# Performance work log

Hardware: AMD Instinct MI355X
Metric: run time of the kernel (lower is better)

## Reference

```python
import jax, jax.numpy as jnp
import numpy as np

M1, M2, BS = 2000, 400, 8
AT = M1 + M2
E1, E2, E3 = 60000, 20000, 20000
H, F, NG, L, C = 64, 64, 50, 4, 4
CUTOFF = 10.0
LOG2 = 0.6931471805599453  # shift of ShiftedSoftplus


def _ssp(x):
    return jax.nn.softplus(x) - LOG2


def _smear(d):
    # GaussianSmearing(0, cutoff, NG)
    offset = jnp.linspace(0.0, CUTOFF, NG)
    coeff = -0.5 / (offset[1] - offset[0]) ** 2
    return jnp.exp(coeff * (d[:, None] - offset[None, :]) ** 2)  # [E, NG]


def _colored_mlp(attr, colors, w1, b1, w2, b2):
    # w1:[C,NG,F] b1:[C,F] w2:[C,F,F] b2:[C,F]; route each edge through its color's MLP
    out = jnp.zeros((attr.shape[0], w1.shape[-1]), attr.dtype)
    for c in range(C):  # fixed small color count
        h = _ssp(attr @ w1[c] + b1[c]) @ w2[c] + b2[c]
        out = out + jnp.where((colors == c)[:, None], h, jnp.zeros((), attr.dtype))
    return out


def _block(h, ei, ew, attr, col, p):
    # InteractionBlock: CFConv -> ssp -> linear
    mw1, mb1, mw2, mb2, cw1, cw2, cb2, bw, bb = p
    Ccut = 0.5 * (jnp.cos(ew * jnp.pi / CUTOFF) + 1.0)
    W = _colored_mlp(attr, col, mw1, mb1, mw2, mb2) * Ccut[:, None]  # [E,F]
    x = h @ cw1                                   # lin1 (no bias) [N,F]
    msg = x[ei[:, 0]] * W                         # gather x_j, modulate
    agg = jax.ops.segment_sum(msg, ei[:, 1], num_segments=h.shape[0])  # scatter-add
    x = agg @ cw2 + cb2                           # lin2
    return _ssp(x) @ bw + bb                      # act + block linear


def _batch_graph(ei, ew, col):
    # replicate per-structure edges across the batch with node offset b*AT
    offs = (jnp.arange(BS, dtype=ei.dtype) * AT)[:, None, None]
    ei_b = (ei[None] + offs).reshape(-1, 2)
    return ei_b, jnp.tile(ew, BS), jnp.tile(col, BS)


def _forward(sites, sites_p, e1, ew1, c1, e2, ew2, c2, e3, ew3, c3,
             emb_w, emb_p_w, mlp_w1, mlp_b1, mlp_w2, mlp_b2,
             conv_w1, conv_w2, conv_b2, blk_w, blk_b,
             out_w1, out_b1, out_w2, out_b2):
    h = jnp.concatenate([emb_w[sites], emb_p_w[sites_p]], axis=1).reshape(BS * AT, H)
    graphs = []
    for (ei, ew, col) in ((e1, ew1, c1), (e2, ew2, c2), (e3, ew3, c3)):
        ei_b, ew_b, col_b = _batch_graph(ei, ew, col)
        graphs.append((ei_b, ew_b, col_b, _smear(ew_b)))
    for l in range(L):
        delta = jnp.zeros_like(h)
        for g, (ei_b, ew_b, col_b, attr_b) in enumerate(graphs):
            p = (mlp_w1[l, g], mlp_b1[l, g], mlp_w2[l, g], mlp_b2[l, g],
                 conv_w1[l, g], conv_w2[l, g], conv_b2[l, g], blk_w[l, g], blk_b[l, g])
            delta = delta + _block(h, ei_b, ew_b, attr_b, col_b, p)
        h = h + delta
    hp = h.reshape(BS, AT, H)[:, M1:, :]   # mask selects pore nodes only
    o = hp @ out_w1 + out_b1               # NB: original has `h - self.act(h)` no-op, so no activation here
    o = o @ out_w2 + out_b2                # [BS, M2, 1]
    return o.sum(axis=1)                   # 'add' readout per batch -> [BS, 1]


def setup_inputs() -> dict:
    key = jax.random.key(0)
    ks = jax.random.split(key, 24)
    f = lambda i, shape, s=0.1: jax.random.normal(ks[i], shape, jnp.float32) * s
    sites = jax.random.randint(ks[0], (BS, M1), 0, 1, dtype=jnp.int32)
    sites_p = jax.random.randint(ks[1], (BS, M2), 0, 2, dtype=jnp.int32)
    e1 = jax.random.randint(ks[2], (E1, 2), 0, M1, dtype=jnp.int32)
    e2 = jnp.stack([jax.random.randint(ks[3], (E2,), 0, M1, dtype=jnp.int32),
                    jax.random.randint(ks[4], (E2,), M1, AT, dtype=jnp.int32)], 1)
    e3 = jnp.stack([jax.random.randint(ks[5], (E3,), M1, AT, dtype=jnp.int32),
                    jax.random.randint(ks[6], (E3,), 0, M1, dtype=jnp.int32)], 1)
    ew1 = jax.random.uniform(ks[7], (E1,), jnp.float32, 0.5, CUTOFF)
    ew2 = jax.random.uniform(ks[8], (E2,), jnp.float32, 0.5, CUTOFF)
    ew3 = jax.random.uniform(ks[9], (E3,), jnp.float32, 0.5, CUTOFF)
    c1 = jax.random.randint(ks[10], (E1,), 0, C, dtype=jnp.int32)
    c2 = jax.random.randint(ks[11], (E2,), 0, C, dtype=jnp.int32)
    c3 = jax.random.randint(ks[12], (E3,), 0, C, dtype=jnp.int32)
    return {
        'sites': sites, 'sites_p': sites_p,
        'edge_idx1': e1, 'edge_weight1': ew1, 'colors1': c1,
        'edge_idx2': e2, 'edge_weight2': ew2, 'colors2': c2,
        'edge_idx3': e3, 'edge_weight3': ew3, 'colors3': c3,
        'emb_w': f(13, (1, H), 1.0), 'emb_p_w': f(14, (2, H), 1.0),
        'mlp_w1': f(15, (L, 3, C, NG, F)), 'mlp_b1': jnp.zeros((L, 3, C, F), jnp.float32),
        'mlp_w2': f(16, (L, 3, C, F, F)), 'mlp_b2': jnp.zeros((L, 3, C, F), jnp.float32),
        'conv_w1': f(17, (L, 3, H, F)), 'conv_w2': f(18, (L, 3, F, H)),
        'conv_b2': jnp.zeros((L, 3, H), jnp.float32),
        'blk_w': f(19, (L, 3, H, H)), 'blk_b': jnp.zeros((L, 3, H), jnp.float32),
        'out_w1': f(20, (H, H // 2)), 'out_b1': jnp.zeros((H // 2,), jnp.float32),
        'out_w2': f(21, (H // 2, 1)), 'out_b2': jnp.zeros((1,), jnp.float32),
    }


def reference(sites, sites_p, edge_idx1, edge_weight1, colors1,
              edge_idx2, edge_weight2, colors2, edge_idx3, edge_weight3, colors3,
              emb_w, emb_p_w, mlp_w1, mlp_b1, mlp_w2, mlp_b2,
              conv_w1, conv_w2, conv_b2, blk_w, blk_b,
              out_w1, out_b1, out_w2, out_b2):
    return _forward(sites, sites_p, edge_idx1, edge_weight1, colors1,
                    edge_idx2, edge_weight2, colors2, edge_idx3, edge_weight3, colors3,
                    emb_w, emb_p_w, mlp_w1, mlp_b1, mlp_w2, mlp_b2,
                    conv_w1, conv_w2, conv_b2, blk_w, blk_b,
                    out_w1, out_b1, out_w2, out_b2)
```

## Files before the change

kernel.cpp:

```cpp
#include <hip/hip_runtime.h>
#include <math.h>

constexpr int M1 = 2000, M2 = 400, BS = 8;
constexpr int AT = M1 + M2;
constexpr int NN = BS * AT;
constexpr int E1 = 60000, E2 = 20000, E3 = 20000;
constexpr int ET = E1 + E2 + E3;
constexpr int H = 64, F = 64, NG = 50, L = 4, C = 4;
constexpr float CUTOFF = 10.0f;
constexpr float LOG2F_ = 0.6931471805599453f;

constexpr float SMEAR_STEP = 10.0f / 49.0f;
constexpr float SMEAR_COEFF = -12.005f;
constexpr float PI_OVER_CUT = 0.31415926535897932f;

constexpr int NBLK = (ET + 255) / 256;

constexpr int NT = 512;
constexpr float DSCALE = (float)(NT - 1) / CUTOFF;

constexpr int TILE_M = 32;
constexpr int MT = NN / TILE_M;

constexpr int NB0 = M1 / 4;
constexpr int NB1 = M2 / 4;
constexpr int NB2 = M1 / 4;
constexpr int NBTOT = NB0 + NB1 + NB2;

constexpr size_t O_HA    = 0;
constexpr size_t O_HB    = O_HA  + (size_t)NN * 64 * 4;
constexpr size_t O_XG    = O_HB  + (size_t)NN * 64 * 4;
constexpr size_t O_DG    = O_XG  + (size_t)3 * AT * 512 * 2;
constexpr size_t O_TAB2  = O_DG  + (size_t)3 * NN * 64 * 4;
constexpr size_t O_EDATA = O_TAB2 + (size_t)48 * NT * 64 * 8;
constexpr size_t O_INT   = O_EDATA + (size_t)ET * 16;
constexpr int I_DEG  = 0;
constexpr int I_CUR  = 7200;
constexpr int I_ZEND = 14400;
constexpr int I_BASE = 14400;
constexpr int I_PERM = 21616;

__device__ inline float sspf(float x) {
    return fmaxf(x, 0.0f) + log1pf(expf(-fabsf(x))) - LOG2F_;
}
__device__ inline float sspf_fast(float x) {
    float t = __expf(-fabsf(x));
    return fmaxf(x, 0.0f) + __logf(1.0f + t) - LOG2F_;
}

__device__ inline unsigned int bf16rn(float x) {
    unsigned int u = __float_as_uint(x);
    u = (u + 0x7FFFu + ((u >> 16) & 1u)) >> 16;
    return u & 0xFFFFu;
}

__device__ inline int graph_off(int g) { return g == 0 ? 0 : (g == 1 ? E1 : E1 + E2); }

__device__ inline void edge_decode(int idx, int& g, int& e,
                                   const int* ei1, const int* ei2, const int* ei3,
                                   const int* c1, const int* c2, const int* c3,
                                   const int*& ei, const int*& cl) {
    if (idx < E1)            { g = 0; e = idx;           ei = ei1; cl = c1; }
    else if (idx < E1 + E2)  { g = 1; e = idx - E1;      ei = ei2; cl = c2; }
    else                     { g = 2; e = idx - E1 - E2; ei = ei3; cl = c3; }
}

__global__ void k_init_h(const int* __restrict__ sites, const int* __restrict__ sites_p,
                         const float* __restrict__ emb_w, const float* __restrict__ emb_p_w,
                         float* __restrict__ h) {
    int idx = blockIdx.x * blockDim.x + threadIdx.x;
    if (idx >= NN * 64) return;
    int f = idx & 63;
    int n = idx >> 6;
    int b = n / AT;
    int i = n - b * AT;
    float v;
    if (i < M1) v = emb_w[sites[b * M1 + i] * H + f];
    else        v = emb_p_w[sites_p[b * M2 + (i - M1)] * H + f];
    h[idx] = v;
}

__global__ void k_count(const int* __restrict__ ei1, const int* __restrict__ ei2,
                        const int* __restrict__ ei3, const int* __restrict__ c1,
                        const int* __restrict__ c2, const int* __restrict__ c3,
                        int* __restrict__ deg) {
    int idx = blockIdx.x * blockDim.x + threadIdx.x;
    if (idx >= ET) return;
    int g, e; const int* ei; const int* cl;
    edge_decode(idx, g, e, ei1, ei2, ei3, c1, c2, c3, ei, cl);
    atomicAdd(&deg[g * AT + ei[2 * e + 1]], 1);
}

__global__ void k_scan(const int* __restrict__ deg, int* __restrict__ base) {
    const int T = 256, CH = 10;
    int t = threadIdx.x;
    __shared__ int lsum[T];
    int g = blockIdx.x;
    int loc[CH];
    int s = 0;
    #pragma unroll
    for (int i = 0; i < CH; i++) {
        int idx = t * CH + i;
        int v = (idx < AT) ? deg[g * AT + idx] : 0;
        loc[i] = s;
        s += v;
    }
    lsum[t] = s;
    __syncthreads();
    for (int off = 1; off < T; off <<= 1) {
        int v = 0;
        if (t >= off) v = lsum[t - off];
        __syncthreads();
        lsum[t] += v;
        __syncthreads();
    }
    int tb = lsum[t] - s;
    #pragma unroll
    for (int i = 0; i < CH; i++) {
        int idx = t * CH + i;
        if (idx < AT) base[g * (AT + 1) + idx] = tb + loc[i];
    }
    if (t == T - 1) base[g * (AT + 1) + AT] = lsum[T - 1];
}

__global__ void k_sort(const int* __restrict__ deg, int* __restrict__ perm) {
    __shared__ int hist[256];
    __shared__ int cur[256];
    int g = blockIdx.x, t = threadIdx.x;
    int off   = (g == 1) ? M1 : 0;
    int cnt   = (g == 1) ? M2 : M1;
    int pbase = (g == 0) ? 0 : ((g == 1) ? M1 : (M1 + M2));
    hist[t] = 0;
    __syncthreads();
    for (int i = t; i < cnt; i += 256)
        atomicAdd(&hist[min(deg[g * AT + off + i], 255)], 1);
    __syncthreads();
    if (t == 0) {
        int run = 0;
        for (int k = 0; k < 256; k++) { cur[k] = run; run += hist[k]; }
    }
    __syncthreads();
    for (int i = t; i < cnt; i += 256) {
        int pos = atomicAdd(&cur[min(deg[g * AT + off + i], 255)], 1);
        perm[pbase + pos] = off + i;
    }
}

__global__ void k_fill(const int* __restrict__ ei1, const int* __restrict__ ei2,
                       const int* __restrict__ ei3, const int* __restrict__ c1,
                       const int* __restrict__ c2, const int* __restrict__ c3,
                       const float* __restrict__ ew1, const float* __restrict__ ew2,
                       const float* __restrict__ ew3,
                       const int* __restrict__ base, int* __restrict__ cur,
                       int4* __restrict__ edata) {
    int idx = blockIdx.x * blockDim.x + threadIdx.x;
    if (idx >= ET) return;
    int g, e; const int* ei; const int* cl;
    edge_decode(idx, g, e, ei1, ei2, ei3, c1, c2, c3, ei, cl);
    const float* ew = (g == 0) ? ew1 : (g == 1 ? ew2 : ew3);
    int dst = ei[2 * e + 1];
    int src = ei[2 * e];
    int p = base[g * (AT + 1) + dst] + atomicAdd(&cur[g * AT + dst], 1);
    float t = ew[e] * DSCALE;
    int i0 = min((int)t, NT - 2);
    float fr = t - (float)i0;
    int cb = cl[e] * (L * NT) + i0;
    edata[graph_off(g) + p] = make_int4(src, cb, __float_as_int(fr), 0);
}

__global__ __launch_bounds__(256) void k_table(
    const float* __restrict__ mlp_w1, const float* __restrict__ mlp_b1,
    const float* __restrict__ mlp_w2, const float* __restrict__ mlp_b2,
    float* __restrict__ tab2) {
    const int lane = threadIdx.x & 63;
    int w = blockIdx.x * 4 + (threadIdx.x >> 6);
    int s = w >> 9;
    int p = w & (NT - 1);
    int l = s % L;
    int gc = s / L;
    int c = gc % C;
    int g = gc / C;
    float d = (float)p * (CUTOFF / (float)(NT - 1));

    size_t wb = (size_t)((l * 3 + g) * C + c);
    const float* w1 = mlp_w1 + wb * NG * F;
    const float* w2 = mlp_w2 + wb * F * F;
    float w1c[NG], w2c[F];
    #pragma unroll
    for (int k = 0; k < NG; k++) w1c[k] = w1[k * F + lane];
    #pragma unroll
    for (int k = 0; k < F; k++) w2c[k] = w2[k * F + lane];
    float b1c = mlp_b1[wb * F + lane];
    float b2c = mlp_b2[wb * F + lane];

    float dd = d - (float)lane * SMEAR_STEP;
    float av = (lane < NG) ? __expf(SMEAR_COEFF * dd * dd) : 0.0f;
    float acc = b1c;
    #pragma unroll
    for (int k = 0; k < NG; k++) acc = fmaf(__shfl(av, k), w1c[k], acc);
    float t = sspf_fast(acc);
    float acc2 = b2c;
    #pragma unroll
    for (int j = 0; j < F; j++) acc2 = fmaf(__shfl(t, j), w2c[j], acc2);
    float ccut = 0.5f * (__cosf(d * PI_OVER_CUT) + 1.0f);
    float val = acc2 * ccut;
    tab2[((size_t)s * NT + p) * 128 + lane * 2] = val;
    if (p > 0)
        tab2[((size_t)s * NT + (p - 1)) * 128 + lane * 2 + 1] = val;
}

__device__ inline void fma4(float acc[4], float a, const float4 b) {
    acc[0] = fmaf(a, b.x, acc[0]);
    acc[1] = fmaf(a, b.y, acc[1]);
    acc[2] = fmaf(a, b.z, acc[2]);
    acc[3] = fmaf(a, b.w, acc[3]);
}

__device__ inline void stage_B(const float* __restrict__ gB, float (*Bs)[68], int t) {
    #pragma unroll
    for (int i = 0; i < 4; i++) {
        int v = t + i * 256;
        int r = v >> 4, c4 = (v & 15) * 4;
        *(float4*)&Bs[r][c4] = *(const float4*)(gB + (size_t)r * 64 + c4);
    }
}
__device__ inline void gemm_tile(const float (*As)[68], const float (*Bs)[68],
                                 int r0, int c0, float acc0[4], float acc1[4]) {
    #pragma unroll 4
    for (int k0 = 0; k0 < 64; k0 += 4) {
        float4 a0 = *(const float4*)&As[r0][k0];
        float4 a1 = *(const float4*)&As[r0 + 1][k0];
        float4 b0 = *(const float4*)&Bs[k0][c0];
        float4 b1 = *(const float4*)&Bs[k0 + 1][c0];
        float4 b2 = *(const float4*)&Bs[k0 + 2][c0];
        float4 b3 = *(const float4*)&Bs[k0 + 3][c0];
        fma4(acc0, a0.x, b0); fma4(acc0, a0.y, b1);
        fma4(acc0, a0.z, b2); fma4(acc0, a0.w, b3);
        fma4(acc1, a1.x, b0); fma4(acc1, a1.y, b1);
        fma4(acc1, a1.z, b2); fma4(acc1, a1.w, b3);
    }
}

__device__ inline void xg_transpose_store(const float (*T)[68],
                                          unsigned short* __restrict__ xg,
                                          int g, int i0, int t) {
    int k = t >> 6, c = t & 63;
    unsigned int w0 = bf16rn(T[k * 8 + 0][c]) | (bf16rn(T[k * 8 + 1][c]) << 16);
    unsigned int w1 = bf16rn(T[k * 8 + 2][c]) | (bf16rn(T[k * 8 + 3][c]) << 16);
    unsigned int w2 = bf16rn(T[k * 8 + 4][c]) | (bf16rn(T[k * 8 + 5][c]) << 16);
    unsigned int w3 = bf16rn(T[k * 8 + 6][c]) | (bf16rn(T[k * 8 + 7][c]) << 16);
    unsigned short* out = xg + (((size_t)g * AT + i0 + k) * 64 + c) * 8;
    *(uint4*)out = make_uint4(w0, w1, w2, w3);
}

__global__ __launch_bounds__(256) void k_lin1t(
    const float* __restrict__ h, const float* __restrict__ conv_w1,
    unsigned short* __restrict__ xg, int l) {
    __shared__ float As[TILE_M][68];
    __shared__ float Bs[64][68];
    int t = threadIdx.x;
    int g = blockIdx.x / MT;
    int igrp = blockIdx.x - g * MT;
    int i0 = igrp * 4;
    #pragma unroll
    for (int it = 0; it < 2; it++) {
        int v = t + it * 256;
        int r = v >> 4, c4 = (v & 15) * 4;
        int n = (r & 7) * AT + i0 + (r >> 3);
        *(float4*)&As[r][c4] = *(const float4*)(h + (size_t)n * 64 + c4);
    }
    stage_B(conv_w1 + (size_t)(l * 3 + g) * 4096, Bs, t);
    __syncthreads();
    int cg = t & 15, rg = t >> 4;
    int c0 = cg * 4, r0 = rg * 2;
    float acc0[4] = {0, 0, 0, 0}, acc1[4] = {0, 0, 0, 0};
    gemm_tile(As, Bs, r0, c0, acc0, acc1);
    __syncthreads();
    *(float4*)&As[r0][c0]     = make_float4(acc0[0], acc0[1], acc0[2], acc0[3]);
    *(float4*)&As[r0 + 1][c0] = make_float4(acc1[0], acc1[1], acc1[2], acc1[3]);
    __syncthreads();
    xg_transpose_store(As, xg, g, i0, t);
}

__global__ __launch_bounds__(256) void k_aggl(
    const int4* __restrict__ edata, const int* __restrict__ base,
    const int* __restrict__ perm,
    const unsigned short* __restrict__ xg, const float* __restrict__ tab2,
    const float* __restrict__ conv_w2, const float* __restrict__ conv_b2,
    const float* __restrict__ blk_w, const float* __restrict__ blk_b,
    float* __restrict__ dg, int l) {
    __shared__ float As[TILE_M][68];
    __shared__ float Bs[64][68];
    int t = threadIdx.x;
    const int lane = t & 63;
    const int wv = t >> 6;
    int bid = blockIdx.x;
    int g, grp, nbg, pbase;
    if (bid < NB0)            { g = 0; grp = bid;             nbg = NB0; pbase = 0; }
    else if (bid < NB0 + NB1) { g = 1; grp = bid - NB0;       nbg = NB1; pbase = M1; }
    else                      { g = 2; grp = bid - NB0 - NB1; nbg = NB2; pbase = M1 + M2; }
    int gi = nbg - 1 - grp;
    int dst = perm[pbase + gi * 4 + wv];
    size_t pb = (size_t)(l * 3 + g);
    stage_B(conv_w2 + pb * 4096, Bs, t);

    const int4* ed = edata + graph_off(g);
    int s = base[g * (AT + 1) + dst];
    int e = base[g * (AT + 1) + dst + 1];
    const float2* tg = (const float2*)tab2 +
                       ((size_t)g * C * L * NT + (size_t)l * NT) * 64;
    const unsigned short* xgg = xg + (size_t)g * AT * 512;
    float acc[8];
    #pragma unroll
    for (int j = 0; j < 8; j++) acc[j] = 0.0f;

    int i = s;
    while (i < e) {
        int cnt = min(e - i, 64);
        int4 mrec = ed[i + min(lane, cnt - 1)];
        int j = 0;
        for (; j + 2 <= cnt; j += 2) {
            int x0 = __shfl(mrec.x, j),     y0 = __shfl(mrec.y, j),     z0 = __shfl(mrec.z, j);
            int x1 = __shfl(mrec.x, j + 1), y1 = __shfl(mrec.y, j + 1), z1 = __shfl(mrec.z, j + 1);
            float2 rv0 = tg[(size_t)y0 * 64 + lane];
            float2 rv1 = tg[(size_t)y1 * 64 + lane];
            uint4 q0 = *(const uint4*)(xgg + ((size_t)x0 * 64 + lane) * 8);
            uint4 q1 = *(const uint4*)(xgg + ((size_t)x1 * 64 + lane) * 8);
            float wl0 = fmaf(__int_as_float(z0), rv0.y - rv0.x, rv0.x);
            float wl1 = fmaf(__int_as_float(z1), rv1.y - rv1.x, rv1.x);
            acc[0] = fmaf(__uint_as_float(q0.x << 16),         wl0, acc[0]);
            acc[1] = fmaf(__uint_as_float(q0.x & 0xFFFF0000u), wl0, acc[1]);
            acc[2] = fmaf(__uint_as_float(q0.y << 16),         wl0, acc[2]);
            acc[3] = fmaf(__uint_as_float(q0.y & 0xFFFF0000u), wl0, acc[3]);
            acc[4] = fmaf(__uint_as_float(q0.z << 16),         wl0, acc[4]);
            acc[5] = fmaf(__uint_as_float(q0.z & 0xFFFF0000u), wl0, acc[5]);
            acc[6] = fmaf(__uint_as_float(q0.w << 16),         wl0, acc[6]);
            acc[7] = fmaf(__uint_as_float(q0.w & 0xFFFF0000u), wl0, acc[7]);
            acc[0] = fmaf(__uint_as_float(q1.x << 16),         wl1, acc[0]);
            acc[1] = fmaf(__uint_as_float(q1.x & 0xFFFF0000u), wl1, acc[1]);
            acc[2] = fmaf(__uint_as_float(q1.y << 16),         wl1, acc[2]);
            acc[3] = fmaf(__uint_as_float(q1.y & 0xFFFF0000u), wl1, acc[3]);
            acc[4] = fmaf(__uint_as_float(q1.z << 16),         wl1, acc[4]);
            acc[5] = fmaf(__uint_as_float(q1.z & 0xFFFF0000u), wl1, acc[5]);
            acc[6] = fmaf(__uint_as_float(q1.w << 16),         wl1, acc[6]);
            acc[7] = fmaf(__uint_as_float(q1.w & 0xFFFF0000u), wl1, acc[7]);
        }
        if (j < cnt) {
            int x0 = __shfl(mrec.x, j), y0 = __shfl(mrec.y, j), z0 = __shfl(mrec.z, j);
            float2 rv = tg[(size_t)y0 * 64 + lane];
            float wl = fmaf(__int_as_float(z0), rv.y - rv.x, rv.x);
            uint4 q = *(const uint4*)(xgg + ((size_t)x0 * 64 + lane) * 8);
            acc[0] = fmaf(__uint_as_float(q.x << 16),         wl, acc[0]);
            acc[1] = fmaf(__uint_as_float(q.x & 0xFFFF0000u), wl, acc[1]);
            acc[2] = fmaf(__uint_as_float(q.y << 16),         wl, acc[2]);
            acc[3] = fmaf(__uint_as_float(q.y & 0xFFFF0000u), wl, acc[3]);
            acc[4] = fmaf(__uint_as_float(q.z << 16),         wl, acc[4]);
            acc[5] = fmaf(__uint_as_float(q.z & 0xFFFF0000u), wl, acc[5]);
            acc[6] = fmaf(__uint_as_float(q.w << 16),         wl, acc[6]);
            acc[7] = fmaf(__uint_as_float(q.w & 0xFFFF0000u), wl, acc[7]);
        }
        i += cnt;
    }
    #pragma unroll
    for (int b2 = 0; b2 < 8; b2++) As[wv * 8 + b2][lane] = acc[b2];
    __syncthreads();

    int cg = t & 15, rg = t >> 4;
    int cc0 = cg * 4, r0 = rg * 2;
    float4 bias = *(const float4*)(conv_b2 + pb * 64 + cc0);
    float a0[4] = {bias.x, bias.y, bias.z, bias.w};
    float a1[4] = {bias.x, bias.y, bias.z, bias.w};
    gemm_tile(As, Bs, r0, cc0, a0, a1);
    __syncthreads();
    *(float4*)&As[r0][cc0] =
        make_float4(sspf(a0[0]), sspf(a0[1]), sspf(a0[2]), sspf(a0[3]));
    *(float4*)&As[r0 + 1][cc0] =
        make_float4(sspf(a1[0]), sspf(a1[1]), sspf(a1[2]), sspf(a1[3]));
    stage_B(blk_w + pb * 4096, Bs, t);
    __syncthreads();
    float4 bb = *(const float4*)(blk_b + pb * 64 + cc0);
    float b0[4] = {bb.x, bb.y, bb.z, bb.w};
    float b1[4] = {bb.x, bb.y, bb.z, bb.w};
    gemm_tile(As, Bs, r0, cc0, b0, b1);
    int dstR = perm[pbase + gi * 4 + (r0 >> 3)];
    float* dp0 = dg + ((size_t)g * NN + (size_t)(r0 & 7) * AT + dstR) * 64 + cc0;
    float* dp1 = dg + ((size_t)g * NN + (size_t)((r0 + 1) & 7) * AT + dstR) * 64 + cc0;
    *(float4*)dp0 = make_float4(b0[0], b0[1], b0[2], b0[3]);
    *(float4*)dp1 = make_float4(b1[0], b1[1], b1[2], b1[3]);
}

__global__ __launch_bounds__(256) void k_lin1f(
    const float* __restrict__ hIn, float* __restrict__ hOut,
    const float* __restrict__ dg, const float* __restrict__ conv_w1,
    const float* __restrict__ conv_b2, const float* __restrict__ blk_w,
    const float* __restrict__ blk_b,
    unsigned short* __restrict__ xg, int lcur, int last) {
    __shared__ float As[TILE_M][68];
    __shared__ float Bs[64][68];
    __shared__ float cv[3][64];
    int t = threadIdx.x;
    int g, igrp;
    if (last) { g = 0; igrp = blockIdx.x; }
    else      { g = blockIdx.x / MT; igrp = blockIdx.x - g * MT; }
    int i0 = igrp * 4;
    int wvi = t >> 6, lane = t & 63;
    if (wvi < 3) {
        size_t pbg = (size_t)(lcur * 3 + wvi);
        float sl = sspf(conv_b2[pbg * 64 + lane]);
        const float* bw = blk_w + pbg * 4096;
        float a = blk_b[pbg * 64 + lane];
        #pragma unroll 8
        for (int k = 0; k < 64; k++)
            a = fmaf(__shfl(sl, k), bw[k * 64 + lane], a);
        cv[wvi][lane] = a;
    }
    __syncthreads();
    #pragma unroll
    for (int it = 0; it < 2; it++) {
        int v = t + it * 256;
        int r = v >> 4, c4 = (v & 15) * 4;
        int k = r >> 3, b = r & 7;
        int node_i = i0 + k;
        size_t o = ((size_t)b * AT + node_i) * 64 + c4;
        float4 hv = *(const float4*)(hIn + o);
        if (node_i < M1) {
            float4 d0 = *(const float4*)(dg + o);
            float4 d2 = *(const float4*)(dg + (size_t)2 * NN * 64 + o);
            float4 c1v = *(const float4*)&cv[1][c4];
            hv.x += d0.x + c1v.x + d2.x;
            hv.y += d0.y + c1v.y + d2.y;
            hv.z += d0.z + c1v.z + d2.z;
            hv.w += d0.w + c1v.w + d2.w;
        } else {
            float4 d1 = *(const float4*)(dg + (size_t)NN * 64 + o);
            float4 c0v = *(const float4*)&cv[0][c4];
            float4 c2v = *(const float4*)&cv[2][c4];
            hv.x += c0v.x + d1.x + c2v.x;
            hv.y += c0v.y + d1.y + c2v.y;
            hv.z += c0v.z + d1.z + c2v.z;
            hv.w += c0v.w + d1.w + c2v.w;
        }
        *(float4*)&As[r][c4] = hv;
        if (g == 0) *(float4*)(hOut + o) = hv;
    }
    if (last) return;
    stage_B(conv_w1 + (size_t)((lcur + 1) * 3 + g) * 4096, Bs, t);
    __syncthreads();
    int cg = t & 15, rg = t >> 4;
    int c0 = cg * 4, r0 = rg * 2;
    float acc0[4] = {0, 0, 0, 0}, acc1[4] = {0, 0, 0, 0};
    gemm_tile(As, Bs, r0, c0, acc0, acc1);
    __syncthreads();
    *(float4*)&As[r0][c0]     = make_float4(acc0[0], acc0[1], acc0[2], acc0[3]);
    *(float4*)&As[r0 + 1][c0] = make_float4(acc1[0], acc1[1], acc1[2], acc1[3]);
    __syncthreads();
    xg_transpose_store(As, xg, g, i0, t);
}

__global__ void k_read(const float* __restrict__ h,
                       const float* __restrict__ w1, const float* __restrict__ b1,
                       const float* __restrict__ w2, const float* __restrict__ b2,
                       float* __restrict__ out) {
    int b = blockIdx.x;
    int lane = threadIdx.x & 63;
    int wv = threadIdx.x >> 6;
    __shared__ float part[4];
    float weff = 0.0f;
    #pragma unroll
    for (int j = 0; j < H / 2; j++) weff = fmaf(w1[lane * (H / 2) + j], w2[j], weff);
    float acc = 0.0f;
    for (int i = wv * (M2 / 4); i < (wv + 1) * (M2 / 4); i++)
        acc += h[((size_t)b * AT + M1 + i) * H + lane];
    float v = acc * weff;
    for (int off = 32; off; off >>= 1) v += __shfl_xor(v, off);
    if (lane == 0) part[wv] = v;
    __syncthreads();
    if (threadIdx.x == 0) {
        float bias = b2[0];
        for (int j = 0; j < H / 2; j++) bias = fmaf(b1[j], w2[j], bias);
        out[b] = part[0] + part[1] + part[2] + part[3] + (float)M2 * bias;
    }
}

extern "C" void kernel_launch(void* const* d_in, const int* in_sizes, int n_in,
                              void* d_out, int out_size, void* d_ws, size_t ws_size,
                              hipStream_t stream) {
    const int* sites   = (const int*)d_in[0];
    const int* sites_p = (const int*)d_in[1];
    const int* ei1 = (const int*)d_in[2];
    const float* ew1 = (const float*)d_in[3];
    const int* c1 = (const int*)d_in[4];
    const int* ei2 = (const int*)d_in[5];
    const float* ew2 = (const float*)d_in[6];
    const int* c2 = (const int*)d_in[7];
    const int* ei3 = (const int*)d_in[8];
    const float* ew3 = (const float*)d_in[9];
    const int* c3 = (const int*)d_in[10];
    const float* emb_w   = (const float*)d_in[11];
    const float* emb_p_w = (const float*)d_in[12];
    const float* mlp_w1 = (const float*)d_in[13];
    const float* mlp_b1 = (const float*)d_in[14];
    const float* mlp_w2 = (const float*)d_in[15];
    const float* mlp_b2 = (const float*)d_in[16];
    const float* conv_w1 = (const float*)d_in[17];
    const float* conv_w2 = (const float*)d_in[18];
    const float* conv_b2 = (const float*)d_in[19];
    const float* blk_w = (const float*)d_in[20];
    const float* blk_b = (const float*)d_in[21];
    const float* out_w1 = (const float*)d_in[22];
    const float* out_b1 = (const float*)d_in[23];
    const float* out_w2 = (const float*)d_in[24];
    const float* out_b2 = (const float*)d_in[25];

    char* ws = (char*)d_ws;
    float* hA   = (float*)(ws + O_HA);
    float* hB   = (float*)(ws + O_HB);
    unsigned short* xg = (unsigned short*)(ws + O_XG);
    float* dg   = (float*)(ws + O_DG);
    float* tab2 = (float*)(ws + O_TAB2);
    int4*  edata = (int4*)(ws + O_EDATA);
    int* ip    = (int*)(ws + O_INT);
    int* deg   = ip + I_DEG;
    int* cur   = ip + I_CUR;
    int* ibase = ip + I_BASE;
    int* dperm = ip + I_PERM;

    hipMemsetAsync(ip, 0, (size_t)I_ZEND * sizeof(int), stream);

    k_table<<<48 * NT / 4, 256, 0, stream>>>(mlp_w1, mlp_b1, mlp_w2, mlp_b2, tab2);
    k_init_h<<<(NN * 64 + 255) / 256, 256, 0, stream>>>(sites, sites_p, emb_w, emb_p_w, hA);
    k_count<<<NBLK, 256, 0, stream>>>(ei1, ei2, ei3, c1, c2, c3, deg);
    k_scan<<<3, 256, 0, stream>>>(deg, ibase);
    k_sort<<<3, 256, 0, stream>>>(deg, dperm);
    k_fill<<<NBLK, 256, 0, stream>>>(ei1, ei2, ei3, c1, c2, c3, ew1, ew2, ew3,
                                     ibase, cur, edata);

    k_lin1t<<<3 * MT, 256, 0, stream>>>(hA, conv_w1, xg, 0);
    float* hcur = hA;
    float* hnxt = hB;
    for (int l = 0; l < L; l++) {
        int last = (l == L - 1) ? 1 : 0;
        k_aggl<<<NBTOT, 256, 0, stream>>>(edata, ibase, dperm, xg, tab2,
                                          conv_w2, conv_b2, blk_w, blk_b,
                                          dg, l);
        k_lin1f<<<last ? MT : 3 * MT, 256, 0, stream>>>(hcur, hnxt, dg, conv_w1,
                                                        conv_b2, blk_w, blk_b,
                                                        xg, l, last);
        float* tmp = hcur; hcur = hnxt; hnxt = tmp;
    }
    k_read<<<BS, 256, 0, stream>>>(hcur, out_w1, out_b1, out_w2, out_b2, (float*)d_out);
}
```

Baseline: 365.1 us.

## Pack filter table as bf16 pairs and restrict lin1 to source nodes needed

The filter lookup table is now computed in fp32 into a scratch buffer, then packed by a new kernel into one 32-bit word per entry holding the bf16 values at points p and p+1. This halves the gather bytes per edge in the aggregation loop. The lin1 transform launches now cover only the node ranges each graph actually reads as sources (M1, M1, M2 groups) instead of all nodes for all three graphs. The h-write condition is adjusted so every node is still written. The cost is an extra launch and bf16 rounding of the filter values.

```diff
diff --git a/kernel.cpp b/kernel.cpp
--- a/kernel.cpp
+++ b/kernel.cpp
@@ -26,6 +26,11 @@
 constexpr int NB1 = M2 / 4;
 constexpr int NB2 = M1 / 4;
 constexpr int NBTOT = NB0 + NB1 + NB2;
+
+constexpr int LT0 = M1 / 4;
+constexpr int LT1 = M1 / 4;
+constexpr int LT2 = M2 / 4;
+constexpr int LTOT = LT0 + LT1 + LT2;
 
 constexpr size_t O_HA    = 0;
 constexpr size_t O_HB    = O_HA  + (size_t)NN * 64 * 4;
@@ -171,7 +176,7 @@
 __global__ __launch_bounds__(256) void k_table(
     const float* __restrict__ mlp_w1, const float* __restrict__ mlp_b1,
     const float* __restrict__ mlp_w2, const float* __restrict__ mlp_b2,
-    float* __restrict__ tab2) {
+    float* __restrict__ tabF) {
     const int lane = threadIdx.x & 63;
     int w = blockIdx.x * 4 + (threadIdx.x >> 6);
     int s = w >> 9;
@@ -203,10 +208,17 @@
     #pragma unroll
     for (int j = 0; j < F; j++) acc2 = fmaf(__shfl(t, j), w2c[j], acc2);
     float ccut = 0.5f * (__cosf(d * PI_OVER_CUT) + 1.0f);
-    float val = acc2 * ccut;
-    tab2[((size_t)s * NT + p) * 128 + lane * 2] = val;
-    if (p > 0)
-        tab2[((size_t)s * NT + (p - 1)) * 128 + lane * 2 + 1] = val;
+    tabF[((size_t)s * NT + p) * 64 + lane] = acc2 * ccut;
+}
+
+__global__ void k_pack(const float* __restrict__ tabF,
+                       unsigned int* __restrict__ tab2) {
+    int idx = blockIdx.x * 256 + threadIdx.x;
+    int pc = idx & (NT * 64 - 1);
+    int nxt = (pc < (NT - 1) * 64) ? idx + 64 : idx;
+    unsigned int lo = bf16rn(tabF[idx]);
+    unsigned int hi = bf16rn(tabF[nxt]);
+    tab2[idx] = lo | (hi << 16);
 }
 
 __device__ inline void fma4(float acc[4], float a, const float4 b) {
@@ -253,14 +265,20 @@
     *(uint4*)out = make_uint4(w0, w1, w2, w3);
 }
 
+__device__ inline void lin1_map(int bid, int& g, int& igrp) {
+    if (bid < LT0)            { g = 0; igrp = bid; }
+    else if (bid < LT0 + LT1) { g = 1; igrp = bid - LT0; }
+    else                      { g = 2; igrp = LT0 + (bid - LT0 - LT1); }
+}
+
 __global__ __launch_bounds__(256) void k_lin1t(
     const float* __restrict__ h, const float* __restrict__ conv_w1,
     unsigned short* __restrict__ xg, int l) {
     __shared__ float As[TILE_M][68];
     __shared__ float Bs[64][68];
     int t = threadIdx.x;
-    int g = blockIdx.x / MT;
-    int igrp = blockIdx.x - g * MT;
+    int g, igrp;
+    lin1_map(blockIdx.x, g, igrp);
     int i0 = igrp * 4;
     #pragma unroll
     for (int it = 0; it < 2; it++) {
@@ -285,7 +303,7 @@
 __global__ __launch_bounds__(256) void k_aggl(
     const int4* __restrict__ edata, const int* __restrict__ base,
     const int* __restrict__ perm,
-    const unsigned short* __restrict__ xg, const float* __restrict__ tab2,
+    const unsigned short* __restrict__ xg, const unsigned int* __restrict__ tab2,
     const float* __restrict__ conv_w2, const float* __restrict__ conv_b2,
     const float* __restrict__ blk_w, const float* __restrict__ blk_b,
     float* __restrict__ dg, int l) {
@@ -307,8 +325,7 @@
     const int4* ed = edata + graph_off(g);
     int s = base[g * (AT + 1) + dst];
     int e = base[g * (AT + 1) + dst + 1];
-    const float2* tg = (const float2*)tab2 +
-                       ((size_t)g * C * L * NT + (size_t)l * NT) * 64;
+    const unsigned int* tg = tab2 + ((size_t)g * C * L * NT + (size_t)l * NT) * 64;
     const unsigned short* xgg = xg + (size_t)g * AT * 512;
     float acc[8];
     #pragma unroll
@@ -322,12 +339,16 @@
         for (; j + 2 <= cnt; j += 2) {
             int x0 = __shfl(mrec.x, j),     y0 = __shfl(mrec.y, j),     z0 = __shfl(mrec.z, j);
             int x1 = __shfl(mrec.x, j + 1), y1 = __shfl(mrec.y, j + 1), z1 = __shfl(mrec.z, j + 1);
-            float2 rv0 = tg[(size_t)y0 * 64 + lane];
-            float2 rv1 = tg[(size_t)y1 * 64 + lane];
+            unsigned int u0 = tg[(size_t)y0 * 64 + lane];
+            unsigned int u1 = tg[(size_t)y1 * 64 + lane];
             uint4 q0 = *(const uint4*)(xgg + ((size_t)x0 * 64 + lane) * 8);
             uint4 q1 = *(const uint4*)(xgg + ((size_t)x1 * 64 + lane) * 8);
-            float wl0 = fmaf(__int_as_float(z0), rv0.y - rv0.x, rv0.x);
-            float wl1 = fmaf(__int_as_float(z1), rv1.y - rv1.x, rv1.x);
+            float lo0 = __uint_as_float(u0 << 16);
+            float hi0 = __uint_as_float(u0 & 0xFFFF0000u);
+            float lo1 = __uint_as_float(u1 << 16);
+            float hi1 = __uint_as_float(u1 & 0xFFFF0000u);
+            float wl0 = fmaf(__int_as_float(z0), hi0 - lo0, lo0);
+            float wl1 = fmaf(__int_as_float(z1), hi1 - lo1, lo1);
             acc[0] = fmaf(__uint_as_float(q0.x << 16),         wl0, acc[0]);
             acc[1] = fmaf(__uint_as_float(q0.x & 0xFFFF0000u), wl0, acc[1]);
             acc[2] = fmaf(__uint_as_float(q0.y << 16),         wl0, acc[2]);
@@ -347,9 +368,11 @@
         }
         if (j < cnt) {
             int x0 = __shfl(mrec.x, j), y0 = __shfl(mrec.y, j), z0 = __shfl(mrec.z, j);
-            float2 rv = tg[(size_t)y0 * 64 + lane];
-            float wl = fmaf(__int_as_float(z0), rv.y - rv.x, rv.x);
+            unsigned int u0 = tg[(size_t)y0 * 64 + lane];
             uint4 q = *(const uint4*)(xgg + ((size_t)x0 * 64 + lane) * 8);
+            float lo0 = __uint_as_float(u0 << 16);
+            float hi0 = __uint_as_float(u0 & 0xFFFF0000u);
+            float wl = fmaf(__int_as_float(z0), hi0 - lo0, lo0);
             acc[0] = fmaf(__uint_as_float(q.x << 16),         wl, acc[0]);
             acc[1] = fmaf(__uint_as_float(q.x & 0xFFFF0000u), wl, acc[1]);
             acc[2] = fmaf(__uint_as_float(q.y << 16),         wl, acc[2]);
@@ -401,8 +424,9 @@
     int t = threadIdx.x;
     int g, igrp;
     if (last) { g = 0; igrp = blockIdx.x; }
-    else      { g = blockIdx.x / MT; igrp = blockIdx.x - g * MT; }
+    else      lin1_map(blockIdx.x, g, igrp);
     int i0 = igrp * 4;
+    int writeH = last ? 1 : (g != 1);
     int wvi = t >> 6, lane = t & 63;
     if (wvi < 3) {
         size_t pbg = (size_t)(lcur * 3 + wvi);
@@ -441,7 +465,7 @@
             hv.w += c0v.w + d1.w + c2v.w;
         }
         *(float4*)&As[r][c4] = hv;
-        if (g == 0) *(float4*)(hOut + o) = hv;
+        if (writeH) *(float4*)(hOut + o) = hv;
     }
     if (last) return;
     stage_B(conv_w1 + (size_t)((lcur + 1) * 3 + g) * 4096, Bs, t);
@@ -517,7 +541,7 @@
     float* hB   = (float*)(ws + O_HB);
     unsigned short* xg = (unsigned short*)(ws + O_XG);
     float* dg   = (float*)(ws + O_DG);
-    float* tab2 = (float*)(ws + O_TAB2);
+    unsigned int* tab2 = (unsigned int*)(ws + O_TAB2);
     int4*  edata = (int4*)(ws + O_EDATA);
     int* ip    = (int*)(ws + O_INT);
     int* deg   = ip + I_DEG;
@@ -527,7 +551,8 @@
 
     hipMemsetAsync(ip, 0, (size_t)I_ZEND * sizeof(int), stream);
 
-    k_table<<<48 * NT / 4, 256, 0, stream>>>(mlp_w1, mlp_b1, mlp_w2, mlp_b2, tab2);
+    k_table<<<48 * NT / 4, 256, 0, stream>>>(mlp_w1, mlp_b1, mlp_w2, mlp_b2, dg);
+    k_pack<<<48 * NT * 64 / 256, 256, 0, stream>>>(dg, tab2);
     k_init_h<<<(NN * 64 + 255) / 256, 256, 0, stream>>>(sites, sites_p, emb_w, emb_p_w, hA);
     k_count<<<NBLK, 256, 0, stream>>>(ei1, ei2, ei3, c1, c2, c3, deg);
     k_scan<<<3, 256, 0, stream>>>(deg, ibase);
@@ -535,7 +560,7 @@
     k_fill<<<NBLK, 256, 0, stream>>>(ei1, ei2, ei3, c1, c2, c3, ew1, ew2, ew3,
                                      ibase, cur, edata);
 
-    k_lin1t<<<3 * MT, 256, 0, stream>>>(hA, conv_w1, xg, 0);
+    k_lin1t<<<LTOT, 256, 0, stream>>>(hA, conv_w1, xg, 0);
     float* hcur = hA;
     float* hnxt = hB;
     for (int l = 0; l < L; l++) {
@@ -543,9 +568,9 @@
         k_aggl<<<NBTOT, 256, 0, stream>>>(edata, ibase, dperm, xg, tab2,
                                           conv_w2, conv_b2, blk_w, blk_b,
                                           dg, l);
-        k_lin1f<<<last ? MT : 3 * MT, 256, 0, stream>>>(hcur, hnxt, dg, conv_w1,
-                                                        conv_b2, blk_w, blk_b,
-                                                        xg, l, last);
+        k_lin1f<<<last ? MT : LTOT, 256, 0, stream>>>(hcur, hnxt, dg, conv_w1,
+                                                      conv_b2, blk_w, blk_b,
+                                                      xg, l, last);
         float* tmp = hcur; hcur = hnxt; hnxt = tmp;
     }
     k_read<<<BS, 256, 0, stream>>>(hcur, out_w1, out_b1, out_w2, out_b2, (float*)d_out);
```

Result: faster. 357.1 us (-2.2%).
